# Kernel tuning notes

Measured on AMD Instinct MI355X. Metric: run time of the kernel, lower is better.

The kernel has to match this reference:

```python
import jax, jax.numpy as jnp
import numpy as np

N_MICS = 8
MIC_RADIUS = 0.05
SAMPLE_RATE = 16000.0
SPEED_SOUND = 343.0
EPS = 1e-20
SPHERE_LEVELS = 4


def sphere_np(levels=SPHERE_LEVELS):
    # Faithful numpy port of the torch icosphere subdivision in sphere().
    h = 5.0 ** 0.5 / 5.0
    r = 2.0 / 5.0 * 5.0 ** 0.5
    pi = 3.141592654
    pts = np.zeros((12, 3), dtype=np.float32)
    pts[0] = [0.0, 0.0, 1.0]
    pts[11] = [0.0, 0.0, -1.0]
    k = np.arange(5, dtype=np.float32)
    pts[1:6, 0] = r * np.sin(2.0 * pi * k / 5.0)
    pts[1:6, 1] = r * np.cos(2.0 * pi * k / 5.0)
    pts[1:6, 2] = h
    pts[6:11, 0] = -r * np.sin(2.0 * pi * k / 5.0)
    pts[6:11, 1] = -r * np.cos(2.0 * pi * k / 5.0)
    pts[6:11, 2] = -h
    trs = np.array([[0, 2, 1], [0, 3, 2], [0, 4, 3], [0, 5, 4], [0, 1, 5],
                    [9, 1, 2], [10, 2, 3], [6, 3, 4], [7, 4, 5], [8, 5, 1],
                    [4, 7, 6], [5, 8, 7], [1, 9, 8], [2, 10, 9], [3, 6, 10],
                    [11, 6, 7], [11, 7, 8], [11, 8, 9], [11, 9, 10], [11, 10, 6]], dtype=np.int64)
    for _ in range(levels):
        T = trs.shape[0]
        sub = np.zeros((4 * T, 6), dtype=np.int64)
        sub[0 * T:1 * T] = trs[:, [0, 0, 0, 1, 2, 0]]
        sub[1 * T:2 * T] = trs[:, [0, 1, 1, 1, 1, 2]]
        sub[2 * T:3 * T] = trs[:, [2, 0, 1, 2, 2, 2]]
        sub[3 * T:4 * T] = trs[:, [0, 1, 1, 2, 2, 0]]
        flat = np.concatenate((sub[:, [0, 1]], sub[:, [2, 3]], sub[:, [4, 5]]), axis=0)
        srt = np.sort(flat, axis=1)
        m = srt.max()
        scal = srt[:, 0] * (m + 1) + srt[:, 1]
        uniq, inv = np.unique(scal, return_inverse=True)
        uv0 = uniq // (m + 1)
        uv1 = uniq - uv0 * (m + 1)
        trs = inv.reshape(3, -1).T
        pts = pts[uv0] + pts[uv1]
        pts /= np.sqrt((pts ** 2).sum(axis=1, keepdims=True))
    return pts.astype(np.float32)


def setup_inputs() -> dict:
    key = jax.random.key(0)
    # DOA grid and TDOAs from array geometry (precomputed in SrpPhat.__init__)
    doas_np = sphere_np()                                    # [2562, 3]
    ang = 2.0 * np.pi * np.arange(N_MICS) / N_MICS
    mics_np = np.stack([MIC_RADIUS * np.cos(ang), MIC_RADIUS * np.sin(ang),
                        np.zeros(N_MICS)], axis=1).astype(np.float32)  # [8, 3]
    taus_np = (SAMPLE_RATE / SPEED_SOUND) * (doas_np @ mics_np.T)      # [2562, 8]
    B, T, F, P = 4, 250, 513, N_MICS * (N_MICS + 1) // 2
    XXs = jax.random.normal(key, (B, T, F, 2, P), dtype=jnp.float32)
    return {"XXs": XXs, "taus": jnp.asarray(taus_np), "doas": jnp.asarray(doas_np)}


def reference(XXs, taus, doas):
    B, T, F, _, P = XXs.shape
    n_mics = taus.shape[1]
    D = taus.shape[0]
    frame_size = (F - 1) * 2
    # Steering phases: a = exp(-j * omega * tau)   [D, F, M]
    omegas = 2.0 * jnp.pi * jnp.arange(F, dtype=jnp.float32) / frame_size
    phase = omegas[None, :, None] * taus[:, None, :]
    A_re = jnp.cos(phase)
    A_im = -jnp.sin(phase)
    # Cross steering terms for every mic pair (triu incl. diagonal): W = a_i * conj(a_j)^H form
    i0, i1 = np.triu_indices(n_mics)                         # 36 pairs for 8 mics
    Ws_re = A_re[:, :, i0] * A_re[:, :, i1] + A_im[:, :, i0] * A_im[:, :, i1]  # [D, F, P]
    Ws_im = A_re[:, :, i0] * A_im[:, :, i1] - A_im[:, :, i0] * A_re[:, :, i1]
    # PHAT normalization of the cross-spectra
    XX_re = XXs[:, :, :, 0, :]
    XX_im = XXs[:, :, :, 1, :]
    mag = jnp.sqrt(XX_re ** 2 + XX_im ** 2) + EPS
    Xr = (XX_re / mag).reshape(B, T, F * P)
    Xi = (XX_im / mag).reshape(B, T, F * P)
    Wr = Ws_re.reshape(D, F * P)
    Wi = Ws_im.reshape(D, F * P)
    # SRP map: Re{ sum_fp XX_norm * conj(W) } reduced over freqs and pairs
    Ys = jnp.matmul(Xr, Wr.T) + jnp.matmul(Xi, Wi.T)         # [B, T, D]
    idx = jnp.argmax(Ys, axis=2)                             # [B, T]
    return doas[idx]                                         # [B, T, 3]
```

## Files before the change

### kernel.cpp

```cpp
#include <hip/hip_runtime.h>
#include <math.h>


#define F_BINS  513
#define M_TOTAL 1000
#define D_TOTAL 2562
#define D_PAD   2688
#define NPAIR   28
#define NC      32
#define K2      (NPAIR * NC)
#define S_SCALE 4.67f
#define NBT     4
#define CNT     8
#define FSPLIT  6
#define KSPB    2
#define KPS     448
#define BT_PAD  1024

#define OFF_COEF 0
#define OFF_TT   16512
#define OFF_GT   (OFF_TT + (size_t)K2 * D_PAD)
#define OFF_GP   (OFF_GT + (size_t)K2 * BT_PAD)
#define OFF_YS   OFF_GP

__device__ __constant__ int c_ptab[NPAIR] = {1,2,3,4,5,6,7, 9,10,11,12,13,14,
                                             16,17,18,19,20, 22,23,24,25,
                                             27,28,29, 31,32, 34};
__device__ __constant__ int c_i0[NPAIR] = {0,0,0,0,0,0,0, 1,1,1,1,1,1,
                                           2,2,2,2,2, 3,3,3,3, 4,4,4, 5,5, 6};
__device__ __constant__ int c_i1[NPAIR] = {1,2,3,4,5,6,7, 2,3,4,5,6,7,
                                           3,4,5,6,7, 4,5,6,7, 5,6,7, 6,7, 7};
__device__ __constant__ int c_inv[36] = {
    -1, 0, 1, 2, 3, 4, 5, 6,
    -1, 7, 8, 9,10,11,12,
    -1,13,14,15,16,17,
    -1,18,19,20,21,
    -1,22,23,24,
    -1,25,26,
    -1,27,
    -1};

__global__ void k_coef(float* __restrict__ coefEO) {
    __shared__ double sHC[NC][NC + 1];
    __shared__ double sHS[NC][NC + 1];
    const int f = blockIdx.x;
    const int t = threadIdx.x;
    const double z = (double)f * (M_PI / 512.0) * (double)S_SCALE;
    double th = M_PI * (t + 0.5) / NC;
    double ct = cos(th);
    double hs, hc;
    sincos(z * ct, &hs, &hc);
    double cp = 1.0, cc = ct, c2 = 2.0 * ct;
    sHC[0][t] = hc;      sHS[0][t] = hs;
    sHC[1][t] = hc * cc; sHS[1][t] = hs * cc;
    for (int n = 2; n < NC; ++n) {
        double cn = c2 * cc - cp;
        cp = cc; cc = cn;
        sHC[n][t] = hc * cn;
        sHS[n][t] = hs * cn;
    }
    __syncthreads();
    const int n = (t < 16) ? 2 * t : 2 * (t - 16) + 1;
    double sum = 0.0;
    if (t < 16) { for (int j = 0; j < NC; ++j) sum += sHC[n][j]; }
    else        { for (int j = 0; j < NC; ++j) sum += sHS[n][j]; }
    double scale = (n == 0) ? (1.0 / NC) : (2.0 / NC);
    coefEO[f * 32 + t] = (float)(sum * scale);
}

__global__ void k_ttab(const float* __restrict__ taus, float* __restrict__ Tt) {
    const int d = blockIdx.x * 256 + threadIdx.x;
    const int p = blockIdx.y;
    if (d >= D_PAD) return;
    const bool live = d < D_TOTAL;
    const int dd = live ? d : 0;
    const float u = (taus[dd * 8 + c_i0[p]] - taus[dd * 8 + c_i1[p]]) * (1.0f / S_SCALE);
    float* base = Tt + (size_t)p * 32 * D_PAD + d;
    base[0] = live ? 1.f : 0.f;
    base[(size_t)16 * D_PAD] = live ? u : 0.f;
    float tp = 1.f, tc = u;
    const float u2 = 2.f * u;
    for (int n = 2; n < NC; ++n) {
        float tn = u2 * tc - tp;
        tp = tc; tc = tn;
        int c = (n & 1) ? 16 + (n >> 1) : (n >> 1);
        base[(size_t)c * D_PAD] = live ? tn : 0.f;
    }
}

#define NSLOT 3
__global__ __launch_bounds__(128, 3) void k_stageA(
    const float* __restrict__ XXs, const float* __restrict__ coefEO,
    float* __restrict__ Gp)
{
    __shared__ float4 sXn4[NBT][CNT / 4][64];
    __shared__ float  sCall[88][32];
    const int t     = threadIdx.x;
    const int bt0   = blockIdx.x * NBT;
    const int split = blockIdx.y;
    const int fbeg  = (F_BINS * split) / FSPLIT;
    const int fend  = (F_BINS * (split + 1)) / FSPLIT;
    const int nf    = fend - fbeg;
    const int p   = t & 31;
    const int sel = t >> 5;
    const bool im = sel >= 2;
    const int row = (p < NPAIR ? p : NPAIR - 1) + (im ? 32 : 0);
    const int c0  = (sel & 1) * 8 + (im ? 16 : 0);

    for (int e = t; e < 88 * 8; e += 128) {
        int fl = e >> 3, q = e & 7;
        int f  = fbeg + fl; if (f > F_BINS - 1) f = F_BINS - 1;
        *(float4*)&sCall[fl][q * 4] = *(const float4*)&coefEO[f * 32 + q * 4];
    }

    float acc[NBT][8] = {};
    float4 cur_re[NSLOT], cur_im[NSLOT], nxt_re[NSLOT], nxt_im[NSLOT];

    auto issue = [&](int fc, float4* vre, float4* vim) {
        const int cnt = min(CNT, fend - fc);
        #pragma unroll
        for (int s = 0; s < NSLOT; ++s) {
            int e = t + s * 128;
            float4 z4 = {0.f, 0.f, 0.f, 0.f};
            vre[s] = z4; vim[s] = z4;
            if (e < NBT * CNT * 9) {
                int q   = e % 9;
                int rbf = e / 9;
                int bt  = rbf / CNT;
                int fl  = rbf - bt * CNT;
                if (fl < cnt) {
                    const float* bp = XXs + (((size_t)(bt0 + bt) * F_BINS) + fc + fl) * 72;
                    vre[s] = *(const float4*)&bp[q * 4];
                    vim[s] = *(const float4*)&bp[36 + q * 4];
                }
            }
        }
    };

    issue(fbeg, cur_re, cur_im);

    for (int fc = fbeg; fc < fend; fc += CNT) {
        __syncthreads();
        #pragma unroll
        for (int s = 0; s < NSLOT; ++s) {
            int e = t + s * 128;
            if (e >= NBT * CNT * 9) break;
            int q   = e % 9;
            int rbf = e / 9;
            int bt  = rbf / CNT;
            int fl  = rbf - bt * CNT;
            float* dst = (float*)&sXn4[bt][fl >> 2][0];
            const float* xr4 = (const float*)&cur_re[s];
            const float* xi4 = (const float*)&cur_im[s];
            #pragma unroll
            for (int j = 0; j < 4; ++j) {
                int pp = c_inv[q * 4 + j];
                if (pp >= 0) {
                    float xr = xr4[j], xi = xi4[j];
                    float inv = 1.f / (sqrtf(xr * xr + xi * xi) + 1e-20f);
                    dst[pp * 4 + (fl & 3)]        = xr * inv;
                    dst[(32 + pp) * 4 + (fl & 3)] = xi * inv;
                }
            }
        }
        if (fc + CNT < fend) issue(fc + CNT, nxt_re, nxt_im);
        __syncthreads();
        const int cbase = fc - fbeg;
        #pragma unroll
        for (int fg = 0; fg < CNT / 4; ++fg) {
            float4 cjA[4], cjB[4];
            #pragma unroll
            for (int j = 0; j < 4; ++j) {
                cjA[j] = *(const float4*)&sCall[cbase + fg * 4 + j][c0];
                cjB[j] = *(const float4*)&sCall[cbase + fg * 4 + j][c0 + 4];
            }
            #pragma unroll
            for (int bt = 0; bt < NBT; ++bt) {
                float4 a4 = sXn4[bt][fg][row];
                float av[4] = {a4.x, a4.y, a4.z, a4.w};
                #pragma unroll
                for (int j = 0; j < 4; ++j) {
                    acc[bt][0] = fmaf(av[j], cjA[j].x, acc[bt][0]);
                    acc[bt][1] = fmaf(av[j], cjA[j].y, acc[bt][1]);
                    acc[bt][2] = fmaf(av[j], cjA[j].z, acc[bt][2]);
                    acc[bt][3] = fmaf(av[j], cjA[j].w, acc[bt][3]);
                    acc[bt][4] = fmaf(av[j], cjB[j].x, acc[bt][4]);
                    acc[bt][5] = fmaf(av[j], cjB[j].y, acc[bt][5]);
                    acc[bt][6] = fmaf(av[j], cjB[j].z, acc[bt][6]);
                    acc[bt][7] = fmaf(av[j], cjB[j].w, acc[bt][7]);
                }
            }
        }
        #pragma unroll
        for (int s = 0; s < NSLOT; ++s) { cur_re[s] = nxt_re[s]; cur_im[s] = nxt_im[s]; }
    }

    if (p < NPAIR) {
        float* gsp = Gp + (size_t)split * M_TOTAL * K2;
        #pragma unroll
        for (int bt = 0; bt < NBT; ++bt) {
            float* g = gsp + (size_t)(bt0 + bt) * K2 + p * 32 + c0;
            float4 v0 = {acc[bt][0], acc[bt][1], acc[bt][2], acc[bt][3]};
            float4 v1 = {acc[bt][4], acc[bt][5], acc[bt][6], acc[bt][7]};
            *(float4*)&g[0] = v0;
            *(float4*)&g[4] = v1;
        }
    }
}

__global__ void k_reduceG(const float* __restrict__ Gp, float* __restrict__ Gt) {
    const int i = blockIdx.x * 256 + threadIdx.x;
    const size_t MK = (size_t)M_TOTAL * K2;
    if (i < (int)MK) {
        int bt = i / K2, k = i - bt * K2;
        float s = 0.f;
        #pragma unroll
        for (int pl = 0; pl < FSPLIT; ++pl) s += Gp[i + pl * MK];
        Gt[(size_t)k * BT_PAD + bt] = s;
    } else if (i < K2 * BT_PAD) {
        int j = i - (int)MK;
        int btp = j / K2, k = j - btp * K2;
        Gt[(size_t)k * BT_PAD + M_TOTAL + btp] = 0.f;
    }
}

#define BKB 32
__global__ __launch_bounds__(256, 4) void k_gemmB(
    const float* __restrict__ Gt, const float* __restrict__ Tt,
    float* __restrict__ Ysp)
{
    __shared__ float sA[BKB][136];
    __shared__ float sB[BKB][68];
    const int t = threadIdx.x;
    const int row0 = blockIdx.x * 128;
    const int col0 = blockIdx.y * 64;
    const int koff = blockIdx.z * KPS;
    const int tx = t & 15;
    const int ty = t >> 4;
    float acc[8][4] = {};

    for (int k0 = 0; k0 < KPS; k0 += BKB) {
        __syncthreads();
        for (int e = t; e < 1024; e += 256) {
            int kk = e >> 5, r4 = (e & 31) * 4;
            *(float4*)&sA[kk][r4] =
                *(const float4*)&Gt[(size_t)(koff + k0 + kk) * BT_PAD + row0 + r4];
        }
        for (int e = t; e < 512; e += 256) {
            int kk = e >> 4, c4 = (e & 15) * 4;
            *(float4*)&sB[kk][c4] =
                *(const float4*)&Tt[(size_t)(koff + k0 + kk) * D_PAD + col0 + c4];
        }
        __syncthreads();
        #pragma unroll 8
        for (int kk = 0; kk < BKB; ++kk) {
            float4 a0 = *(const float4*)&sA[kk][ty * 8];
            float4 a1 = *(const float4*)&sA[kk][ty * 8 + 4];
            float4 b  = *(const float4*)&sB[kk][tx * 4];
            float av[8] = {a0.x, a0.y, a0.z, a0.w, a1.x, a1.y, a1.z, a1.w};
            float bv[4] = {b.x, b.y, b.z, b.w};
            #pragma unroll
            for (int i = 0; i < 8; ++i)
                #pragma unroll
                for (int j = 0; j < 4; ++j)
                    acc[i][j] = fmaf(av[i], bv[j], acc[i][j]);
        }
    }
    float* yp = Ysp + (size_t)blockIdx.z * M_TOTAL * D_PAD;
    #pragma unroll
    for (int i = 0; i < 8; ++i) {
        int rg = row0 + ty * 8 + i;
        if (rg >= M_TOTAL) continue;
        float4 v = {acc[i][0], acc[i][1], acc[i][2], acc[i][3]};
        *(float4*)(yp + (size_t)rg * D_PAD + col0 + tx * 4) = v;
    }
}

__global__ __launch_bounds__(256) void k_argmax(
    const float* __restrict__ Ysp, const float* __restrict__ doas,
    float* __restrict__ out)
{
    __shared__ float sv[256];
    __shared__ int   si[256];
    const int row = blockIdx.x;
    const int tid = threadIdx.x;
    const float* y0 = Ysp + (size_t)row * D_PAD;
    const float* y1 = y0 + (size_t)M_TOTAL * D_PAD;
    float best = -INFINITY;
    int bi = D_TOTAL;
    for (int d = tid; d < D_TOTAL; d += 256) {
        float v = y0[d] + y1[d];
        if (v > best) { best = v; bi = d; }
    }
    sv[tid] = best; si[tid] = bi;
    __syncthreads();
    for (int s = 128; s > 0; s >>= 1) {
        if (tid < s) {
            float v2 = sv[tid + s]; int i2 = si[tid + s];
            if (v2 > sv[tid] || (v2 == sv[tid] && i2 < si[tid])) { sv[tid] = v2; si[tid] = i2; }
        }
        __syncthreads();
    }
    if (tid == 0) {
        int idx = si[0];
        out[row * 3 + 0] = doas[idx * 3 + 0];
        out[row * 3 + 1] = doas[idx * 3 + 1];
        out[row * 3 + 2] = doas[idx * 3 + 2];
    }
}

extern "C" void kernel_launch(void* const* d_in, const int* in_sizes, int n_in,
                              void* d_out, int out_size, void* d_ws, size_t ws_size,
                              hipStream_t stream) {
    const float* XXs  = (const float*)d_in[0];
    const float* taus = (const float*)d_in[1];
    const float* doas = (const float*)d_in[2];
    float* ws     = (float*)d_ws;
    float* coefEO = ws + OFF_COEF;
    float* Tt     = ws + OFF_TT;
    float* Gt     = ws + OFF_GT;
    float* Gp     = ws + OFF_GP;
    float* Ysp    = ws + OFF_YS;

    k_coef   <<<F_BINS, 32, 0, stream>>>(coefEO);
    k_ttab   <<<dim3((D_PAD + 255) / 256, NPAIR), 256, 0, stream>>>(taus, Tt);
    k_stageA <<<dim3(M_TOTAL / NBT, FSPLIT), 128, 0, stream>>>(XXs, coefEO, Gp);
    k_reduceG<<<(K2 * BT_PAD + 255) / 256, 256, 0, stream>>>(Gp, Gt);
    k_gemmB  <<<dim3(BT_PAD / 128, D_PAD / 64, KSPB), 256, 0, stream>>>(Gt, Tt, Ysp);
    k_argmax <<<M_TOTAL, 256, 0, stream>>>(Ysp, doas, (float*)d_out);
}
```

Measured before the change: 340.9 us.

## Retune splits, precompute stageA indexing, tile reduceG transpose, enlarge GEMM row tile

```diff
diff --git a/kernel.cpp b/kernel.cpp
--- a/kernel.cpp
+++ b/kernel.cpp
@@ -12,9 +12,9 @@
 #define S_SCALE 4.67f
 #define NBT     4
 #define CNT     8
-#define FSPLIT  6
-#define KSPB    2
-#define KPS     448
+#define FSPLIT  12
+#define KSPB    4
+#define KPS     224
 #define BT_PAD  1024
 
 #define OFF_COEF 0
@@ -89,50 +89,65 @@
 }
 
 #define NSLOT 3
-__global__ __launch_bounds__(128, 3) void k_stageA(
+__global__ __launch_bounds__(128, 4) void k_stageA(
     const float* __restrict__ XXs, const float* __restrict__ coefEO,
     float* __restrict__ Gp)
 {
     __shared__ float4 sXn4[NBT][CNT / 4][64];
-    __shared__ float  sCall[88][32];
+    __shared__ float  sCall[48][32];
     const int t     = threadIdx.x;
     const int bt0   = blockIdx.x * NBT;
     const int split = blockIdx.y;
     const int fbeg  = (F_BINS * split) / FSPLIT;
     const int fend  = (F_BINS * (split + 1)) / FSPLIT;
-    const int nf    = fend - fbeg;
     const int p   = t & 31;
     const int sel = t >> 5;
     const bool im = sel >= 2;
     const int row = (p < NPAIR ? p : NPAIR - 1) + (im ? 32 : 0);
     const int c0  = (sel & 1) * 8 + (im ? 16 : 0);
 
-    for (int e = t; e < 88 * 8; e += 128) {
+    for (int e = t; e < 48 * 8; e += 128) {
         int fl = e >> 3, q = e & 7;
         int f  = fbeg + fl; if (f > F_BINS - 1) f = F_BINS - 1;
         *(float4*)&sCall[fl][q * 4] = *(const float4*)&coefEO[f * 32 + q * 4];
     }
 
+    const float* srcs[NSLOT];
+    float*       dstb[NSLOT];
+    int          offj[NSLOT][4];
+    int          flv [NSLOT];
+    #pragma unroll
+    for (int s = 0; s < NSLOT; ++s) {
+        int e    = t + s * 128;
+        bool act = e < NBT * CNT * 9;
+        int ec  = act ? e : 0;
+        int q   = ec % 9;
+        int rbf = ec / 9;
+        int bt  = rbf / CNT;
+        int fl  = rbf - bt * CNT;
+        flv[s]  = act ? fl : 127;
+        srcs[s] = XXs + (((size_t)(bt0 + bt) * F_BINS) + fl) * 72 + q * 4;
+        dstb[s] = (float*)&sXn4[bt][fl >> 2][0] + (fl & 3);
+        #pragma unroll
+        for (int j = 0; j < 4; ++j) {
+            int pp = c_inv[q * 4 + j];
+            offj[s][j] = (act && pp >= 0) ? pp * 4 : -1;
+        }
+    }
+
     float acc[NBT][8] = {};
     float4 cur_re[NSLOT], cur_im[NSLOT], nxt_re[NSLOT], nxt_im[NSLOT];
 
     auto issue = [&](int fc, float4* vre, float4* vim) {
-        const int cnt = min(CNT, fend - fc);
+        const int cnt = fend - fc;
         #pragma unroll
         for (int s = 0; s < NSLOT; ++s) {
-            int e = t + s * 128;
             float4 z4 = {0.f, 0.f, 0.f, 0.f};
             vre[s] = z4; vim[s] = z4;
-            if (e < NBT * CNT * 9) {
-                int q   = e % 9;
-                int rbf = e / 9;
-                int bt  = rbf / CNT;
-                int fl  = rbf - bt * CNT;
-                if (fl < cnt) {
-                    const float* bp = XXs + (((size_t)(bt0 + bt) * F_BINS) + fc + fl) * 72;
-                    vre[s] = *(const float4*)&bp[q * 4];
-                    vim[s] = *(const float4*)&bp[36 + q * 4];
-                }
+            if (flv[s] < cnt) {
+                const float* bp = srcs[s] + (size_t)fc * 72;
+                vre[s] = *(const float4*)bp;
+                vim[s] = *(const float4*)(bp + 36);
             }
         }
     };
@@ -143,23 +158,16 @@
         __syncthreads();
         #pragma unroll
         for (int s = 0; s < NSLOT; ++s) {
-            int e = t + s * 128;
-            if (e >= NBT * CNT * 9) break;
-            int q   = e % 9;
-            int rbf = e / 9;
-            int bt  = rbf / CNT;
-            int fl  = rbf - bt * CNT;
-            float* dst = (float*)&sXn4[bt][fl >> 2][0];
             const float* xr4 = (const float*)&cur_re[s];
             const float* xi4 = (const float*)&cur_im[s];
             #pragma unroll
             for (int j = 0; j < 4; ++j) {
-                int pp = c_inv[q * 4 + j];
-                if (pp >= 0) {
+                int o = offj[s][j];
+                if (o >= 0) {
                     float xr = xr4[j], xi = xi4[j];
-                    float inv = 1.f / (sqrtf(xr * xr + xi * xi) + 1e-20f);
-                    dst[pp * 4 + (fl & 3)]        = xr * inv;
-                    dst[(32 + pp) * 4 + (fl & 3)] = xi * inv;
+                    float inv = rsqrtf(xr * xr + xi * xi + 1e-37f);
+                    dstb[s][o]       = xr * inv;
+                    dstb[s][o + 128] = xi * inv;
                 }
             }
         }
@@ -208,19 +216,33 @@
     }
 }
 
-__global__ void k_reduceG(const float* __restrict__ Gp, float* __restrict__ Gt) {
-    const int i = blockIdx.x * 256 + threadIdx.x;
+__global__ __launch_bounds__(256) void k_reduceG(
+    const float* __restrict__ Gp, float* __restrict__ Gt)
+{
+    __shared__ float sT[32][65];
+    const int t   = threadIdx.x;
+    const int k0  = blockIdx.x * 32;
+    const int bt0 = blockIdx.y * 64;
     const size_t MK = (size_t)M_TOTAL * K2;
-    if (i < (int)MK) {
-        int bt = i / K2, k = i - bt * K2;
+    #pragma unroll
+    for (int i = 0; i < 8; ++i) {
+        int e  = t + i * 256;
+        int kl = e & 31, btl = e >> 5;
+        int bt = bt0 + btl;
         float s = 0.f;
-        #pragma unroll
-        for (int pl = 0; pl < FSPLIT; ++pl) s += Gp[i + pl * MK];
-        Gt[(size_t)k * BT_PAD + bt] = s;
-    } else if (i < K2 * BT_PAD) {
-        int j = i - (int)MK;
-        int btp = j / K2, k = j - btp * K2;
-        Gt[(size_t)k * BT_PAD + M_TOTAL + btp] = 0.f;
+        if (bt < M_TOTAL) {
+            const float* g = Gp + (size_t)bt * K2 + k0 + kl;
+            #pragma unroll
+            for (int pl = 0; pl < FSPLIT; ++pl) s += g[pl * MK];
+        }
+        sT[kl][btl] = s;
+    }
+    __syncthreads();
+    #pragma unroll
+    for (int i = 0; i < 8; ++i) {
+        int e   = t + i * 256;
+        int btl = e & 63, kl = e >> 6;
+        Gt[(size_t)(k0 + kl) * BT_PAD + bt0 + btl] = sT[kl][btl];
     }
 }
 
@@ -229,24 +251,28 @@
     const float* __restrict__ Gt, const float* __restrict__ Tt,
     float* __restrict__ Ysp)
 {
-    __shared__ float sA[BKB][136];
+    __shared__ float sA[BKB][260];
     __shared__ float sB[BKB][68];
     const int t = threadIdx.x;
-    const int row0 = blockIdx.x * 128;
+    const int row0 = blockIdx.x * 256;
     const int col0 = blockIdx.y * 64;
     const int koff = blockIdx.z * KPS;
     const int tx = t & 15;
     const int ty = t >> 4;
-    float acc[8][4] = {};
+    float acc[16][4] = {};
 
     for (int k0 = 0; k0 < KPS; k0 += BKB) {
         __syncthreads();
-        for (int e = t; e < 1024; e += 256) {
-            int kk = e >> 5, r4 = (e & 31) * 4;
+        #pragma unroll
+        for (int i = 0; i < 8; ++i) {
+            int e = t + i * 256;
+            int kk = e >> 6, r4 = (e & 63) * 4;
             *(float4*)&sA[kk][r4] =
                 *(const float4*)&Gt[(size_t)(koff + k0 + kk) * BT_PAD + row0 + r4];
         }
-        for (int e = t; e < 512; e += 256) {
+        #pragma unroll
+        for (int i = 0; i < 2; ++i) {
+            int e = t + i * 256;
             int kk = e >> 4, c4 = (e & 15) * 4;
             *(float4*)&sB[kk][c4] =
                 *(const float4*)&Tt[(size_t)(koff + k0 + kk) * D_PAD + col0 + c4];
@@ -254,13 +280,16 @@
         __syncthreads();
         #pragma unroll 8
         for (int kk = 0; kk < BKB; ++kk) {
-            float4 a0 = *(const float4*)&sA[kk][ty * 8];
-            float4 a1 = *(const float4*)&sA[kk][ty * 8 + 4];
             float4 b  = *(const float4*)&sB[kk][tx * 4];
-            float av[8] = {a0.x, a0.y, a0.z, a0.w, a1.x, a1.y, a1.z, a1.w};
+            float4 a0 = *(const float4*)&sA[kk][ty * 16];
+            float4 a1 = *(const float4*)&sA[kk][ty * 16 + 4];
+            float4 a2 = *(const float4*)&sA[kk][ty * 16 + 8];
+            float4 a3 = *(const float4*)&sA[kk][ty * 16 + 12];
+            float av[16] = {a0.x, a0.y, a0.z, a0.w, a1.x, a1.y, a1.z, a1.w,
+                            a2.x, a2.y, a2.z, a2.w, a3.x, a3.y, a3.z, a3.w};
             float bv[4] = {b.x, b.y, b.z, b.w};
             #pragma unroll
-            for (int i = 0; i < 8; ++i)
+            for (int i = 0; i < 16; ++i)
                 #pragma unroll
                 for (int j = 0; j < 4; ++j)
                     acc[i][j] = fmaf(av[i], bv[j], acc[i][j]);
@@ -268,8 +297,8 @@
     }
     float* yp = Ysp + (size_t)blockIdx.z * M_TOTAL * D_PAD;
     #pragma unroll
-    for (int i = 0; i < 8; ++i) {
-        int rg = row0 + ty * 8 + i;
+    for (int i = 0; i < 16; ++i) {
+        int rg = row0 + ty * 16 + i;
         if (rg >= M_TOTAL) continue;
         float4 v = {acc[i][0], acc[i][1], acc[i][2], acc[i][3]};
         *(float4*)(yp + (size_t)rg * D_PAD + col0 + tx * 4) = v;
@@ -284,12 +313,12 @@
     __shared__ int   si[256];
     const int row = blockIdx.x;
     const int tid = threadIdx.x;
-    const float* y0 = Ysp + (size_t)row * D_PAD;
-    const float* y1 = y0 + (size_t)M_TOTAL * D_PAD;
+    const float* y = Ysp + (size_t)row * D_PAD;
+    const size_t PL = (size_t)M_TOTAL * D_PAD;
     float best = -INFINITY;
     int bi = D_TOTAL;
     for (int d = tid; d < D_TOTAL; d += 256) {
-        float v = y0[d] + y1[d];
+        float v = y[d] + y[d + PL] + y[d + 2 * PL] + y[d + 3 * PL];
         if (v > best) { best = v; bi = d; }
     }
     sv[tid] = best; si[tid] = bi;
@@ -325,7 +354,7 @@
     k_coef   <<<F_BINS, 32, 0, stream>>>(coefEO);
     k_ttab   <<<dim3((D_PAD + 255) / 256, NPAIR), 256, 0, stream>>>(taus, Tt);
     k_stageA <<<dim3(M_TOTAL / NBT, FSPLIT), 128, 0, stream>>>(XXs, coefEO, Gp);
-    k_reduceG<<<(K2 * BT_PAD + 255) / 256, 256, 0, stream>>>(Gp, Gt);
-    k_gemmB  <<<dim3(BT_PAD / 128, D_PAD / 64, KSPB), 256, 0, stream>>>(Gt, Tt, Ysp);
+    k_reduceG<<<dim3(K2 / 32, BT_PAD / 64), 256, 0, stream>>>(Gp, Gt);
+    k_gemmB  <<<dim3(BT_PAD / 256, D_PAD / 64, KSPB), 256, 0, stream>>>(Gt, Tt, Ysp);
     k_argmax <<<M_TOTAL, 256, 0, stream>>>(Ysp, doas, (float*)d_out);
 }
```

Measured after the change: 408.6 us. +19.9%, slower.
